# Performance work log

Measured on AMD Instinct MI355X. Metric: run time of the kernel, lower is better.

The kernel has to match this reference:

```python
import jax, jax.numpy as jnp
import numpy as np

NEG_INF = -1e9  # masked_fill value from the torch module


def setup_inputs() -> dict:
    key = jax.random.key(0)
    ks = jax.random.split(key, 6)
    n_edges, hidden = 100000, 256
    n_paths, max_len = 20000, 16
    edge_emb = jax.random.normal(ks[0], (n_edges, hidden), dtype=jnp.float32)
    paths = jax.random.randint(ks[1], (n_paths, max_len), 0, n_edges)
    path_lens = jax.random.randint(ks[2], (n_paths,), 0, max_len)  # +1 in reference -> 1..max_len
    path_mask = jax.random.randint(ks[3], (n_paths,), 0, 2)
    # nn.Linear(hidden, 1) parameters
    W = jax.random.normal(ks[4], (1, hidden), dtype=jnp.float32) / np.sqrt(hidden)
    b = jax.random.normal(ks[5], (1,), dtype=jnp.float32) * 0.01
    return {"edge_emb": edge_emb, "paths": paths, "path_lens": path_lens,
            "path_mask": path_mask, "W": W, "b": b, "deterministic": 1}


def reference(edge_emb, paths, path_lens, path_mask, W, b, deterministic):
    # ragged per-path mean: emulate `for p in paths: edge_emb[p].mean(0)` with padded gather
    lens = path_lens + 1                                   # [P], 1..max_len
    pos = jnp.arange(paths.shape[1])                        # [L]
    valid = pos[None, :] < lens[:, None]                    # [P, L]
    gathered = edge_emb[paths]                              # [P, L, H]
    z = jnp.sum(jnp.where(valid[..., None], gathered, 0.0), axis=1) / lens[:, None].astype(edge_emb.dtype)  # [P, H]
    logits = z @ W[0] + b[0]                                # [P]  (Linear(H,1).squeeze())
    logits = jnp.where(path_mask == 0, NEG_INF, logits)
    logp = jax.nn.log_softmax(logits)
    if deterministic:
        p = jnp.argmax(logits)
    else:
        p = jax.random.categorical(jax.random.key(42), logits)
    logprob = logp[p]
    return (p, logprob, z[p])
```

## Files before the change

kernel.cpp:

```cpp
#include <hip/hip_runtime.h>
#include <math.h>
#include <limits.h>

#define NEG_INF -1e9f


__global__ __launch_bounds__(256) void k_scatter16(
    const int* __restrict__ paths, const int* __restrict__ path_lens,
    const int* __restrict__ path_mask, unsigned char* __restrict__ flags,
    int n_paths)
{
    int t = blockIdx.x * 256 + (int)threadIdx.x;
    if (t >= n_paths * 16) return;
    int p = t >> 4;
    if (path_mask[p] == 0) return;
    if ((t & 15) > path_lens[p]) return;
    flags[paths[t]] = 1;
}

__global__ __launch_bounds__(256) void k_dot_flag(
    const float* __restrict__ emb, const float* __restrict__ W,
    const unsigned char* __restrict__ flags, float* __restrict__ s,
    int n_edges, int n_waves)
{
    int wave = (blockIdx.x * 256 + (int)threadIdx.x) >> 6;
    int lane = threadIdx.x & 63;
    const float4 w4 = ((const float4*)W)[lane];
    for (int e = wave; e < n_edges; e += n_waves) {
        if (!flags[e]) continue;
        float4 r = ((const float4*)emb)[(size_t)e * 64 + lane];
        float d = r.x * w4.x + r.y * w4.y + r.z * w4.z + r.w * w4.w;
#pragma unroll
        for (int off = 32; off; off >>= 1) d += __shfl_down(d, off, 64);
        if (lane == 0) s[e] = d;
    }
}

__global__ __launch_bounds__(1024) void k_fused16(
    const float* __restrict__ s, const int* __restrict__ paths,
    const int* __restrict__ path_lens, const int* __restrict__ path_mask,
    const float* __restrict__ b, const float* __restrict__ emb,
    float* __restrict__ pmax, int* __restrict__ pidx, float* __restrict__ psum,
    int* __restrict__ counter, float* __restrict__ out,
    int n_paths, int max_len)
{
    __shared__ float l_log[64];
    __shared__ int   l_idx[64];
    __shared__ float rv[16]; __shared__ int ri[16]; __shared__ float rs[16];
    __shared__ float s_M, s_S; __shared__ int s_P, s_last;

    const int tid = threadIdx.x, lane = tid & 63, wv = tid >> 6;
    const int t = blockIdx.x * 1024 + tid;
    const int p = t >> 4, slot = t & 15;

    float val = 0.f; int mask = 0, len = 1; const int inb = (p < n_paths);
    if (inb) {
        mask = path_mask[p];
        len  = path_lens[p] + 1;
        if (mask && slot < len) val = s[paths[t]];
    }
#pragma unroll
    for (int m = 1; m <= 8; m <<= 1) val += __shfl_xor(val, m, 16);
    if (slot == 0) {
        l_log[tid >> 4] = inb ? (mask ? val / (float)len + b[0] : NEG_INF)
                              : -INFINITY;
        l_idx[tid >> 4] = inb ? p : INT_MAX;
    }
    __syncthreads();

    if (wv == 0) {
        float v = l_log[lane]; int vi = l_idx[lane];
        float bv = v; int bi = vi;
#pragma unroll
        for (int off = 32; off; off >>= 1) {
            float ov = __shfl_down(bv, off, 64);
            int   oi = __shfl_down(bi, off, 64);
            if (ov > bv || (ov == bv && oi < bi)) { bv = ov; bi = oi; }
        }
        float bm = __shfl(bv, 0, 64);
        float se = expf(v - bm);
#pragma unroll
        for (int off = 32; off; off >>= 1) se += __shfl_down(se, off, 64);
        if (lane == 0) {
            pmax[blockIdx.x] = bv;
            pidx[blockIdx.x] = bi;
            psum[blockIdx.x] = (bi == INT_MAX) ? 0.f : se;
            __threadfence();
            int tk = atomicAdd(counter, 1);
            s_last = (tk == (int)gridDim.x - 1) ? 1 : 0;
        }
    }
    __syncthreads();
    if (!s_last) return;
    __threadfence();

    const int nb = gridDim.x;
    float mv = -INFINITY; int mi = INT_MAX;
    for (int i = tid; i < nb; i += 1024) {
        float tv = pmax[i]; int ti = pidx[i];
        if (tv > mv || (tv == mv && ti < mi)) { mv = tv; mi = ti; }
    }
#pragma unroll
    for (int off = 32; off; off >>= 1) {
        float ov = __shfl_down(mv, off, 64);
        int   oi = __shfl_down(mi, off, 64);
        if (ov > mv || (ov == mv && oi < mi)) { mv = ov; mi = oi; }
    }
    if (lane == 0) { rv[wv] = mv; ri[wv] = mi; }
    __syncthreads();
    if (tid == 0) {
        float M = rv[0]; int P = ri[0];
        for (int w = 1; w < 16; ++w)
            if (rv[w] > M || (rv[w] == M && ri[w] < P)) { M = rv[w]; P = ri[w]; }
        s_M = M; s_P = P;
    }
    __syncthreads();
    const float M = s_M; const int P = s_P;

    float sp = 0.f;
    for (int i = tid; i < nb; i += 1024)
        sp += psum[i] * expf(pmax[i] - M);
#pragma unroll
    for (int off = 32; off; off >>= 1) sp += __shfl_down(sp, off, 64);
    if (lane == 0) rs[wv] = sp;
    __syncthreads();
    if (tid == 0) {
        float tot = 0.f;
        for (int w = 0; w < 16; ++w) tot += rs[w];
        s_S = tot;
    }
    __syncthreads();

    const int lenP = path_lens[P] + 1;
    const int* pp = paths + (size_t)P * max_len;
    if (tid < 256) {
        float acc = 0.f;
        for (int j = 0; j < lenP; ++j)
            acc += emb[(size_t)pp[j] * 256 + tid];
        out[2 + tid] = acc / (float)lenP;
    }
    if (tid == 0) { out[0] = (float)P; out[1] = -logf(s_S); }
}


__global__ __launch_bounds__(256) void k_edge_dot(
    const float* __restrict__ emb, const float* __restrict__ W,
    float* __restrict__ s, int* __restrict__ counter, int n_edges)
{
    if (blockIdx.x == 0 && threadIdx.x == 0) *counter = 0;
    int wave = (blockIdx.x * (int)blockDim.x + (int)threadIdx.x) >> 6;
    int lane = threadIdx.x & 63;
    if (wave >= n_edges) return;
    const float4 e = ((const float4*)emb)[(size_t)wave * 64 + lane];
    const float4 w = ((const float4*)W)[lane];
    float d = e.x * w.x + e.y * w.y + e.z * w.z + e.w * w.w;
#pragma unroll
    for (int off = 32; off; off >>= 1) d += __shfl_down(d, off, 64);
    if (lane == 0) s[wave] = d;
}

__global__ __launch_bounds__(256) void k_fused_gen(
    const float* __restrict__ s, const int* __restrict__ paths,
    const int* __restrict__ path_lens, const int* __restrict__ path_mask,
    const float* __restrict__ b, const float* __restrict__ emb,
    float* __restrict__ pmax, int* __restrict__ pidx, float* __restrict__ psum,
    int* __restrict__ counter, float* __restrict__ out,
    int n_paths, int max_len)
{
    __shared__ float rv[4]; __shared__ int ri[4]; __shared__ float rs[4];
    __shared__ float s_M, s_S; __shared__ int s_P, s_last;

    const int tid = threadIdx.x, lane = tid & 63, wv = tid >> 6;
    const int p = blockIdx.x * 256 + tid;

    float v = -INFINITY; int vi = INT_MAX;
    if (p < n_paths) {
        vi = p;
        if (path_mask[p] == 0) v = NEG_INF;
        else {
            int len = path_lens[p] + 1;
            const int* pp = paths + (size_t)p * max_len;
            float acc = 0.f;
            for (int j = 0; j < len; ++j) acc += s[pp[j]];
            v = acc / (float)len + b[0];
        }
    }
    float bv = v; int bi = vi;
#pragma unroll
    for (int off = 32; off; off >>= 1) {
        float ov = __shfl_down(bv, off, 64);
        int   oi = __shfl_down(bi, off, 64);
        if (ov > bv || (ov == bv && oi < bi)) { bv = ov; bi = oi; }
    }
    if (lane == 0) { rv[wv] = bv; ri[wv] = bi; }
    __syncthreads();
    if (tid == 0) {
        float mvv = rv[0]; int mii = ri[0];
        for (int w = 1; w < 4; ++w)
            if (rv[w] > mvv || (rv[w] == mvv && ri[w] < mii)) { mvv = rv[w]; mii = ri[w]; }
        s_M = mvv; s_P = mii;
    }
    __syncthreads();
    const float bm = s_M;
    float se = expf(v - bm);
#pragma unroll
    for (int off = 32; off; off >>= 1) se += __shfl_down(se, off, 64);
    if (lane == 0) rs[wv] = se;
    __syncthreads();
    if (tid == 0) {
        pmax[blockIdx.x] = bm;
        pidx[blockIdx.x] = s_P;
        psum[blockIdx.x] = rs[0] + rs[1] + rs[2] + rs[3];
        __threadfence();
        int tk = atomicAdd(counter, 1);
        s_last = (tk == (int)gridDim.x - 1) ? 1 : 0;
    }
    __syncthreads();
    if (!s_last) return;
    __threadfence();

    const int nb = gridDim.x;
    float mv = -INFINITY; int mi = INT_MAX;
    for (int i = tid; i < nb; i += 256) {
        float tv = pmax[i]; int ti = pidx[i];
        if (tv > mv || (tv == mv && ti < mi)) { mv = tv; mi = ti; }
    }
#pragma unroll
    for (int off = 32; off; off >>= 1) {
        float ov = __shfl_down(mv, off, 64);
        int   oi = __shfl_down(mi, off, 64);
        if (ov > mv || (ov == mv && oi < mi)) { mv = ov; mi = oi; }
    }
    if (lane == 0) { rv[wv] = mv; ri[wv] = mi; }
    __syncthreads();
    if (tid == 0) {
        float M = rv[0]; int P = ri[0];
        for (int w = 1; w < 4; ++w)
            if (rv[w] > M || (rv[w] == M && ri[w] < P)) { M = rv[w]; P = ri[w]; }
        s_M = M; s_P = P;
    }
    __syncthreads();
    const float M = s_M; const int P = s_P;
    float sp = 0.f;
    for (int i = tid; i < nb; i += 256)
        sp += psum[i] * expf(pmax[i] - M);
#pragma unroll
    for (int off = 32; off; off >>= 1) sp += __shfl_down(sp, off, 64);
    if (lane == 0) rs[wv] = sp;
    __syncthreads();
    if (tid == 0) s_S = rs[0] + rs[1] + rs[2] + rs[3];
    __syncthreads();

    const int lenP = path_lens[P] + 1;
    const int* pp = paths + (size_t)P * max_len;
    if (tid < 256) {
        float acc = 0.f;
        for (int j = 0; j < lenP; ++j)
            acc += emb[(size_t)pp[j] * 256 + tid];
        out[2 + tid] = acc / (float)lenP;
    }
    if (tid == 0) { out[0] = (float)P; out[1] = -logf(s_S); }
}


extern "C" void kernel_launch(void* const* d_in, const int* in_sizes, int n_in,
                              void* d_out, int out_size, void* d_ws, size_t ws_size,
                              hipStream_t stream) {
    const float* emb       = (const float*)d_in[0];
    const int*   paths     = (const int*)  d_in[1];
    const int*   path_lens = (const int*)  d_in[2];
    const int*   path_mask = (const int*)  d_in[3];
    const float* W         = (const float*)d_in[4];
    const float* b         = (const float*)d_in[5];

    int hidden  = in_sizes[4];
    int n_edges = in_sizes[0] / hidden;
    int n_paths = in_sizes[2];
    int max_len = in_sizes[1] / n_paths;

    if (max_len == 16 && hidden == 256) {
        size_t flags_pad = ((size_t)n_edges + 255) & ~(size_t)255;
        unsigned char* flags = (unsigned char*)d_ws;
        int*   counter = (int*)(flags + flags_pad);
        float* s       = (float*)(flags + flags_pad + 256);
        int nb3 = (n_paths * 16 + 1023) / 1024;
        float* pmax = s + n_edges;
        float* psum = pmax + nb3;
        int*   pidx = (int*)(psum + nb3);

        hipMemsetAsync(d_ws, 0, flags_pad + sizeof(int), stream);

        int blocksS = (n_paths * 16 + 255) / 256;
        k_scatter16<<<blocksS, 256, 0, stream>>>(paths, path_lens, path_mask,
                                                 flags, n_paths);

        int blocksD = 4096;
        k_dot_flag<<<blocksD, 256, 0, stream>>>(emb, W, flags, s,
                                                n_edges, blocksD * 4);

        k_fused16<<<nb3, 1024, 0, stream>>>(s, paths, path_lens, path_mask,
                                            b, emb, pmax, pidx, psum, counter,
                                            (float*)d_out, n_paths, max_len);
    } else {
        float* s = (float*)d_ws;
        int blocks2 = (n_paths + 255) / 256;
        float* pmax    = s + n_edges;
        float* psum    = pmax + blocks2;
        int*   pidx    = (int*)(psum + blocks2);
        int*   counter = pidx + blocks2;

        int blocks1 = (n_edges * 64 + 255) / 256;
        k_edge_dot<<<blocks1, 256, 0, stream>>>(emb, W, s, counter, n_edges);
        k_fused_gen<<<blocks2, 256, 0, stream>>>(s, paths, path_lens, path_mask,
                                                 b, emb, pmax, pidx, psum, counter,
                                                 (float*)d_out, n_paths, max_len);
    }
}
```

Measured before the change: 176.1 us.

## Replace flag-scatter sparse dot with dense edge dot and 256-thread slot reduction

Removes the memset, the flag scatter kernel and the flag-gated per-edge dot. Instead it computes the dot product for every edge densely and then runs a 256-thread fused kernel where 16 threads cooperate per path. The intent is to cut the launch count and drop the memset and scatter pass. The cost is reading the full embedding table instead of only the referenced rows, and the final reduction now runs over four times as many block partials.

```diff
diff --git a/kernel.cpp b/kernel.cpp
--- a/kernel.cpp
+++ b/kernel.cpp
@@ -3,145 +3,6 @@
 #include <limits.h>
 
 #define NEG_INF -1e9f
-
-
-__global__ __launch_bounds__(256) void k_scatter16(
-    const int* __restrict__ paths, const int* __restrict__ path_lens,
-    const int* __restrict__ path_mask, unsigned char* __restrict__ flags,
-    int n_paths)
-{
-    int t = blockIdx.x * 256 + (int)threadIdx.x;
-    if (t >= n_paths * 16) return;
-    int p = t >> 4;
-    if (path_mask[p] == 0) return;
-    if ((t & 15) > path_lens[p]) return;
-    flags[paths[t]] = 1;
-}
-
-__global__ __launch_bounds__(256) void k_dot_flag(
-    const float* __restrict__ emb, const float* __restrict__ W,
-    const unsigned char* __restrict__ flags, float* __restrict__ s,
-    int n_edges, int n_waves)
-{
-    int wave = (blockIdx.x * 256 + (int)threadIdx.x) >> 6;
-    int lane = threadIdx.x & 63;
-    const float4 w4 = ((const float4*)W)[lane];
-    for (int e = wave; e < n_edges; e += n_waves) {
-        if (!flags[e]) continue;
-        float4 r = ((const float4*)emb)[(size_t)e * 64 + lane];
-        float d = r.x * w4.x + r.y * w4.y + r.z * w4.z + r.w * w4.w;
-#pragma unroll
-        for (int off = 32; off; off >>= 1) d += __shfl_down(d, off, 64);
-        if (lane == 0) s[e] = d;
-    }
-}
-
-__global__ __launch_bounds__(1024) void k_fused16(
-    const float* __restrict__ s, const int* __restrict__ paths,
-    const int* __restrict__ path_lens, const int* __restrict__ path_mask,
-    const float* __restrict__ b, const float* __restrict__ emb,
-    float* __restrict__ pmax, int* __restrict__ pidx, float* __restrict__ psum,
-    int* __restrict__ counter, float* __restrict__ out,
-    int n_paths, int max_len)
-{
-    __shared__ float l_log[64];
-    __shared__ int   l_idx[64];
-    __shared__ float rv[16]; __shared__ int ri[16]; __shared__ float rs[16];
-    __shared__ float s_M, s_S; __shared__ int s_P, s_last;
-
-    const int tid = threadIdx.x, lane = tid & 63, wv = tid >> 6;
-    const int t = blockIdx.x * 1024 + tid;
-    const int p = t >> 4, slot = t & 15;
-
-    float val = 0.f; int mask = 0, len = 1; const int inb = (p < n_paths);
-    if (inb) {
-        mask = path_mask[p];
-        len  = path_lens[p] + 1;
-        if (mask && slot < len) val = s[paths[t]];
-    }
-#pragma unroll
-    for (int m = 1; m <= 8; m <<= 1) val += __shfl_xor(val, m, 16);
-    if (slot == 0) {
-        l_log[tid >> 4] = inb ? (mask ? val / (float)len + b[0] : NEG_INF)
-                              : -INFINITY;
-        l_idx[tid >> 4] = inb ? p : INT_MAX;
-    }
-    __syncthreads();
-
-    if (wv == 0) {
-        float v = l_log[lane]; int vi = l_idx[lane];
-        float bv = v; int bi = vi;
-#pragma unroll
-        for (int off = 32; off; off >>= 1) {
-            float ov = __shfl_down(bv, off, 64);
-            int   oi = __shfl_down(bi, off, 64);
-            if (ov > bv || (ov == bv && oi < bi)) { bv = ov; bi = oi; }
-        }
-        float bm = __shfl(bv, 0, 64);
-        float se = expf(v - bm);
-#pragma unroll
-        for (int off = 32; off; off >>= 1) se += __shfl_down(se, off, 64);
-        if (lane == 0) {
-            pmax[blockIdx.x] = bv;
-            pidx[blockIdx.x] = bi;
-            psum[blockIdx.x] = (bi == INT_MAX) ? 0.f : se;
-            __threadfence();
-            int tk = atomicAdd(counter, 1);
-            s_last = (tk == (int)gridDim.x - 1) ? 1 : 0;
-        }
-    }
-    __syncthreads();
-    if (!s_last) return;
-    __threadfence();
-
-    const int nb = gridDim.x;
-    float mv = -INFINITY; int mi = INT_MAX;
-    for (int i = tid; i < nb; i += 1024) {
-        float tv = pmax[i]; int ti = pidx[i];
-        if (tv > mv || (tv == mv && ti < mi)) { mv = tv; mi = ti; }
-    }
-#pragma unroll
-    for (int off = 32; off; off >>= 1) {
-        float ov = __shfl_down(mv, off, 64);
-        int   oi = __shfl_down(mi, off, 64);
-        if (ov > mv || (ov == mv && oi < mi)) { mv = ov; mi = oi; }
-    }
-    if (lane == 0) { rv[wv] = mv; ri[wv] = mi; }
-    __syncthreads();
-    if (tid == 0) {
-        float M = rv[0]; int P = ri[0];
-        for (int w = 1; w < 16; ++w)
-            if (rv[w] > M || (rv[w] == M && ri[w] < P)) { M = rv[w]; P = ri[w]; }
-        s_M = M; s_P = P;
-    }
-    __syncthreads();
-    const float M = s_M; const int P = s_P;
-
-    float sp = 0.f;
-    for (int i = tid; i < nb; i += 1024)
-        sp += psum[i] * expf(pmax[i] - M);
-#pragma unroll
-    for (int off = 32; off; off >>= 1) sp += __shfl_down(sp, off, 64);
-    if (lane == 0) rs[wv] = sp;
-    __syncthreads();
-    if (tid == 0) {
-        float tot = 0.f;
-        for (int w = 0; w < 16; ++w) tot += rs[w];
-        s_S = tot;
-    }
-    __syncthreads();
-
-    const int lenP = path_lens[P] + 1;
-    const int* pp = paths + (size_t)P * max_len;
-    if (tid < 256) {
-        float acc = 0.f;
-        for (int j = 0; j < lenP; ++j)
-            acc += emb[(size_t)pp[j] * 256 + tid];
-        out[2 + tid] = acc / (float)lenP;
-    }
-    if (tid == 0) { out[0] = (float)P; out[1] = -logf(s_S); }
-}
-
 
 __global__ __launch_bounds__(256) void k_edge_dot(
     const float* __restrict__ emb, const float* __restrict__ W,
@@ -159,6 +20,100 @@
     if (lane == 0) s[wave] = d;
 }
 
+__global__ __launch_bounds__(256) void k_fused_slot(
+    const float* __restrict__ s, const int* __restrict__ paths,
+    const int* __restrict__ path_lens, const int* __restrict__ path_mask,
+    const float* __restrict__ b, const float* __restrict__ emb,
+    float* __restrict__ pmax, int* __restrict__ pidx, float* __restrict__ psum,
+    int* __restrict__ counter, float* __restrict__ out,
+    int n_paths, int max_len)
+{
+    __shared__ float bl[16];  __shared__ int bix[16];
+    __shared__ float rv[4];   __shared__ int ri[4];   __shared__ float rs[4];
+    __shared__ float s_M, s_S; __shared__ int s_P, s_last;
+
+    const int tid = threadIdx.x, lane = tid & 63, wv = tid >> 6;
+    const int t = blockIdx.x * 256 + tid;
+    const int p = t >> 4, slot = t & 15;
+
+    float val = 0.f; int mask = 0, len = 1;
+    const int inb = (p < n_paths);
+    if (inb) {
+        mask = path_mask[p];
+        len  = path_lens[p] + 1;
+        if (mask && slot < len) val = s[paths[t]];
+    }
+#pragma unroll
+    for (int m = 1; m <= 8; m <<= 1) val += __shfl_xor(val, m, 16);
+    if (slot == 0) {
+        bl[tid >> 4]  = inb ? (mask ? val / (float)len + b[0] : NEG_INF)
+                            : -INFINITY;
+        bix[tid >> 4] = inb ? p : INT_MAX;
+    }
+    __syncthreads();
+
+    if (tid == 0) {
+        float bm = -INFINITY; int bi = INT_MAX;
+        for (int i = 0; i < 16; ++i)
+            if (bl[i] > bm || (bl[i] == bm && bix[i] < bi)) { bm = bl[i]; bi = bix[i]; }
+        float bs = 0.f;
+        if (bi != INT_MAX)
+            for (int i = 0; i < 16; ++i)
+                if (bix[i] != INT_MAX) bs += expf(bl[i] - bm);
+        pmax[blockIdx.x] = bm;
+        pidx[blockIdx.x] = bi;
+        psum[blockIdx.x] = bs;
+        __threadfence();
+        int tk = atomicAdd(counter, 1);
+        s_last = (tk == (int)gridDim.x - 1) ? 1 : 0;
+    }
+    __syncthreads();
+    if (!s_last) return;
+    __threadfence();
+
+    const int nb = gridDim.x;
+    float mv = -INFINITY; int mi = INT_MAX;
+    for (int i = tid; i < nb; i += 256) {
+        float tv = pmax[i]; int ti = pidx[i];
+        if (tv > mv || (tv == mv && ti < mi)) { mv = tv; mi = ti; }
+    }
+#pragma unroll
+    for (int off = 32; off; off >>= 1) {
+        float ov = __shfl_down(mv, off, 64);
+        int   oi = __shfl_down(mi, off, 64);
+        if (ov > mv || (ov == mv && oi < mi)) { mv = ov; mi = oi; }
+    }
+    if (lane == 0) { rv[wv] = mv; ri[wv] = mi; }
+    __syncthreads();
+    if (tid == 0) {
+        float M = rv[0]; int P = ri[0];
+        for (int w = 1; w < 4; ++w)
+            if (rv[w] > M || (rv[w] == M && ri[w] < P)) { M = rv[w]; P = ri[w]; }
+        s_M = M; s_P = P;
+    }
+    __syncthreads();
+    const float M = s_M; const int P = s_P;
+
+    float sp = 0.f;
+    for (int i = tid; i < nb; i += 256)
+        sp += psum[i] * expf(pmax[i] - M);
+#pragma unroll
+    for (int off = 32; off; off >>= 1) sp += __shfl_down(sp, off, 64);
+    if (lane == 0) rs[wv] = sp;
+    __syncthreads();
+    if (tid == 0) s_S = rs[0] + rs[1] + rs[2] + rs[3];
+    __syncthreads();
+
+    const int lenP = path_lens[P] + 1;
+    const int* pp = paths + (size_t)P * max_len;
+    float acc = 0.f;
+    for (int j = 0; j < lenP; ++j)
+        acc += emb[(size_t)pp[j] * 256 + tid];
+    out[2 + tid] = acc / (float)lenP;
+    if (tid == 0) { out[0] = (float)P; out[1] = -logf(s_S); }
+}
+
+
 __global__ __launch_bounds__(256) void k_fused_gen(
     const float* __restrict__ s, const int* __restrict__ paths,
     const int* __restrict__ path_lens, const int* __restrict__ path_mask,
@@ -278,31 +233,21 @@
     int n_paths = in_sizes[2];
     int max_len = in_sizes[1] / n_paths;
 
+    float* s = (float*)d_ws;
+
     if (max_len == 16 && hidden == 256) {
-        size_t flags_pad = ((size_t)n_edges + 255) & ~(size_t)255;
-        unsigned char* flags = (unsigned char*)d_ws;
-        int*   counter = (int*)(flags + flags_pad);
-        float* s       = (float*)(flags + flags_pad + 256);
-        int nb3 = (n_paths * 16 + 1023) / 1024;
-        float* pmax = s + n_edges;
-        float* psum = pmax + nb3;
-        int*   pidx = (int*)(psum + nb3);
-
-        hipMemsetAsync(d_ws, 0, flags_pad + sizeof(int), stream);
-
-        int blocksS = (n_paths * 16 + 255) / 256;
-        k_scatter16<<<blocksS, 256, 0, stream>>>(paths, path_lens, path_mask,
-                                                 flags, n_paths);
-
-        int blocksD = 4096;
-        k_dot_flag<<<blocksD, 256, 0, stream>>>(emb, W, flags, s,
-                                                n_edges, blocksD * 4);
-
-        k_fused16<<<nb3, 1024, 0, stream>>>(s, paths, path_lens, path_mask,
-                                            b, emb, pmax, pidx, psum, counter,
-                                            (float*)d_out, n_paths, max_len);
+        int nb2 = (n_paths * 16 + 255) / 256;
+        float* pmax    = s + n_edges;
+        float* psum    = pmax + nb2;
+        int*   pidx    = (int*)(psum + nb2);
+        int*   counter = pidx + nb2;
+
+        int blocks1 = (n_edges * 64 + 255) / 256;
+        k_edge_dot<<<blocks1, 256, 0, stream>>>(emb, W, s, counter, n_edges);
+        k_fused_slot<<<nb2, 256, 0, stream>>>(s, paths, path_lens, path_mask,
+                                              b, emb, pmax, pidx, psum, counter,
+                                              (float*)d_out, n_paths, max_len);
     } else {
-        float* s = (float*)d_ws;
         int blocks2 = (n_paths + 255) / 256;
         float* pmax    = s + n_edges;
         float* psum    = pmax + blocks2;
```

After: 190.4 us. 1.08x slower.
